# Kernel tuning notes

Measured on AMD Instinct MI355X. Metric: run time of the kernel, lower is better.

The kernel has to match this reference:

```python
import jax, jax.numpy as jnp
import numpy as np

N = 100000          # nodes
E = 1600000         # edges (avg degree 16)
D = 128             # prototype feature dim
C = 100             # num classes
NUM_LAYERS = 3      # propagation layers


def setup_inputs() -> dict:
    key = jax.random.key(0)
    k1, k2, k3, k4 = jax.random.split(key, 4)
    train_mask = jax.random.randint(k1, (N,), 0, 2) > 0                # bool [N]
    labels_all = jax.random.randint(k2, (N,), 0, C)                    # int   [N]
    edge_index = jax.random.randint(k3, (2, E), 0, N)                  # int   [2,E]
    global_protos = jax.random.normal(k4, (C, D), dtype=jnp.float32)   # [C,D]
    alpha = jnp.float32(0.5)                                           # learnable scalar
    return dict(train_mask=train_mask, global_protos=global_protos,
                labels_all=labels_all, edge_index=edge_index, alpha=alpha)


def _label_propagate(y0, edge_index, alpha):
    # symmetric GCN normalization D^-1/2 A D^-1/2 (no self loops), as in PyG LabelPropagation
    src, dst = edge_index[0], edge_index[1]
    deg = jax.ops.segment_sum(jnp.ones((E,), y0.dtype), dst, num_segments=N)
    deg_inv_sqrt = jnp.where(deg > 0, jax.lax.rsqrt(jnp.maximum(deg, 1.0)), 0.0)
    norm = deg_inv_sqrt[src] * deg_inv_sqrt[dst]                       # [E]
    res = (1.0 - alpha) * y0                                           # residual term
    out = y0
    for _ in range(NUM_LAYERS):
        msgs = out[src] * norm[:, None]                                # gather [E,D]
        agg = jax.ops.segment_sum(msgs, dst, num_segments=N)           # scatter-add [N,D]
        out = jnp.clip(alpha * agg + res, 0.0, 1.0)                    # post_step clamp
    return out


def reference(train_mask, global_protos, labels_all, edge_index, alpha):
    # proto_rep[train_mask] = global_protos[labels_all[train_mask]], zeros elsewhere
    y0 = jnp.where(train_mask[:, None], global_protos[labels_all], 0.0)  # [N,D]
    return _label_propagate(y0, edge_index, alpha)
```

## Files before the change

kernel.cpp:

```cpp
#include <hip/hip_runtime.h>
#include <stdint.h>

typedef _Float16 f16;

#define N_NODES 100000
#define N_EDGES 1600000
#define CAP     64
#define NC      196
#define SLOTS   40
#define SEGCAP  12288
#define EPB     4096
#define SPAD    (CAP + 4)


__global__ __launch_bounds__(256) void bin_kernel(
    const int* __restrict__ src, const int* __restrict__ dst,
    int* __restrict__ gcur, unsigned int* __restrict__ gbins) {
    __shared__ int lcnt[NC];
    __shared__ int gb[NC];
    __shared__ unsigned int lbuf[NC * SLOTS];
    int t = threadIdx.x;
    for (int b = t; b < NC; b += 256) lcnt[b] = 0;
    __syncthreads();

    int base = blockIdx.x * EPB;
    int sv[16], dv[16];
#pragma unroll
    for (int k = 0; k < 16; ++k) {
        int i = base + k * 256 + t;
        sv[k] = (i < N_EDGES) ? src[i] : -1;
        dv[k] = (i < N_EDGES) ? dst[i] : 0;
    }
#pragma unroll
    for (int k = 0; k < 16; ++k) {
        if (sv[k] >= 0) {
            int d = dv[k];
            int cb = d >> 9;
            unsigned rec = (unsigned)sv[k] | ((unsigned)(d & 511) << 17);
            int pos = atomicAdd(&lcnt[cb], 1);
            if (pos < SLOTS) {
                lbuf[cb * SLOTS + pos] = rec;
            } else {
                int gp = atomicAdd(&gcur[cb], 1);
                if (gp < SEGCAP) gbins[(size_t)cb * SEGCAP + gp] = rec;
            }
        }
    }
    __syncthreads();
    if (t < NC) {
        int c = lcnt[t]; if (c > SLOTS) c = SLOTS;
        gb[t] = atomicAdd(&gcur[t], c);
    }
    __syncthreads();
    int wave = t >> 6, lane = t & 63;
    for (int b = wave; b < NC; b += 4) {
        int c = lcnt[b]; if (c > SLOTS) c = SLOTS;
        if (lane < c)
            gbins[(size_t)b * SEGCAP + gb[b] + lane] = lbuf[b * SLOTS + lane];
    }
}


__global__ __launch_bounds__(512) void csr_kernel(
    const unsigned int* __restrict__ gbins, const int* __restrict__ gcur,
    int* __restrict__ cnt, int* __restrict__ csr, float* __restrict__ dis,
    const int* __restrict__ mask, const int* __restrict__ labels,
    int* __restrict__ c0, const float* __restrict__ protos,
    f16* __restrict__ pf16) {
    __shared__ int lc[512];
    int b = blockIdx.x;
    int t = threadIdx.x;
    lc[t] = 0;
    __syncthreads();
    int m = gcur[b]; if (m > SEGCAP) m = SEGCAP;
    const unsigned int* seg = gbins + (size_t)b * SEGCAP;
    int base = b << 9;
    for (int i = t; i < m; i += 512) {
        unsigned int v = seg[i];
        int dl = (int)(v >> 17);
        int pos = atomicAdd(&lc[dl], 1);
        if (pos < CAP) csr[(size_t)(base + dl) * CAP + pos] = (int)(v & 0x1FFFF);
    }
    __syncthreads();
    int n = base + t;
    if (n < N_NODES) {
        int d = lc[t];
        cnt[n] = d;
        dis[n] = (d > 0) ? rsqrtf((float)d) : 0.0f;
        c0[n] = mask[n] ? labels[n] : -1;
    }
    if (b < 25) pf16[b * 512 + t] = (f16)protos[b * 512 + t];
}


template <int MODE>
__global__ __launch_bounds__(256) void prop_kernel(
    const void* __restrict__ rows_, void* __restrict__ out,
    const int* __restrict__ cnt, const int* __restrict__ csr,
    const float* __restrict__ dis, const int* __restrict__ c0,
    const float* __restrict__ protos, const float* __restrict__ alpha_p) {
    __shared__ uint2 smeta[4][4][SPAD];
    int t = threadIdx.x;
    int wave = t >> 6, lane = t & 63;
    int grp = lane >> 4, s16 = lane & 15;
    int n = blockIdx.x * 16 + wave * 4 + grp;

    float alpha = *alpha_p;
    int m = cnt[n]; if (m > CAP) m = CAP;
    float dn = dis[n];
    const int* bucket = csr + (size_t)n * CAP;
    const float inv255 = 1.0f / 255.0f;

    int mm = m;
    { int o = __shfl_xor(mm, 16); mm = mm > o ? mm : o;
      o = __shfl_xor(mm, 32);     mm = mm > o ? mm : o; }
    int mp = (mm + 3) & ~3;

    for (int e = s16; e < mp; e += 16) {
        unsigned wb = 0, off = 0;
        if (e < m) {
            int s = bucket[e];
            float w = dis[s] * dn;
            if (MODE == 0) {
                int c = c0[s];
                if (c < 0) w = 0.f; else off = (unsigned)c << 4;
            } else {
                off = (unsigned)s << 4;
                w *= inv255;
            }
            wb = __float_as_uint(w);
        }
        smeta[wave][grp][e] = make_uint2(wb, off);
    }

    const uint4* md = (const uint4*)&smeta[wave][grp][0];
    float acc[8] = {0.f, 0.f, 0.f, 0.f, 0.f, 0.f, 0.f, 0.f};

    if (MODE == 0) {
        const uint4* r4 = (const uint4*)rows_;
        uint4 mA0, mA1, gA0, gA1, gA2, gA3;
        uint4 mB0, mB1, gB0, gB1, gB2, gB3;
#define LOADB(MM0, MM1, G0, G1, G2, G3, J) do {            \
    MM0 = md[(J) >> 1]; MM1 = md[((J) >> 1) + 1];          \
    G0 = r4[MM0.y + s16]; G1 = r4[MM0.w + s16];            \
    G2 = r4[MM1.y + s16]; G3 = r4[MM1.w + s16]; } while (0)
#define COMP1(WB, G) do {                                  \
    union { uint4 u; f16 h[8]; } q_; q_.u = (G);           \
    float w_ = __uint_as_float(WB);                        \
    _Pragma("unroll")                                      \
    for (int i_ = 0; i_ < 8; ++i_)                         \
        acc[i_] = fmaf((float)q_.h[i_], w_, acc[i_]); } while (0)
#define COMP(MM0, MM1, G0, G1, G2, G3) do {                \
    COMP1(MM0.x, G0); COMP1(MM0.z, G1);                    \
    COMP1(MM1.x, G2); COMP1(MM1.z, G3); } while (0)
        if (mp > 0) {
            LOADB(mA0, mA1, gA0, gA1, gA2, gA3, 0);
            for (int j = 0; j < mp; j += 8) {
                if (j + 4 < mp) LOADB(mB0, mB1, gB0, gB1, gB2, gB3, j + 4);
                COMP(mA0, mA1, gA0, gA1, gA2, gA3);
                if (j + 8 < mp) LOADB(mA0, mA1, gA0, gA1, gA2, gA3, j + 8);
                if (j + 4 < mp) COMP(mB0, mB1, gB0, gB1, gB2, gB3);
            }
        }
#undef LOADB
#undef COMP1
#undef COMP
    } else {
        const uint2* r2 = (const uint2*)rows_;
        uint4 mA0, mA1, mB0, mB1;
        uint2 gA0, gA1, gA2, gA3, gB0, gB1, gB2, gB3;
#define LOADB(MM0, MM1, G0, G1, G2, G3, J) do {            \
    MM0 = md[(J) >> 1]; MM1 = md[((J) >> 1) + 1];          \
    G0 = r2[MM0.y + s16]; G1 = r2[MM0.w + s16];            \
    G2 = r2[MM1.y + s16]; G3 = r2[MM1.w + s16]; } while (0)
#define COMP1(WB, G) do {                                  \
    float w_ = __uint_as_float(WB);                        \
    unsigned x_ = (G).x, y_ = (G).y;                       \
    acc[0] = fmaf((float)(x_ & 0xffu),         w_, acc[0]); \
    acc[1] = fmaf((float)((x_ >> 8) & 0xffu),  w_, acc[1]); \
    acc[2] = fmaf((float)((x_ >> 16) & 0xffu), w_, acc[2]); \
    acc[3] = fmaf((float)(x_ >> 24),           w_, acc[3]); \
    acc[4] = fmaf((float)(y_ & 0xffu),         w_, acc[4]); \
    acc[5] = fmaf((float)((y_ >> 8) & 0xffu),  w_, acc[5]); \
    acc[6] = fmaf((float)((y_ >> 16) & 0xffu), w_, acc[6]); \
    acc[7] = fmaf((float)(y_ >> 24),           w_, acc[7]); } while (0)
#define COMP(MM0, MM1, G0, G1, G2, G3) do {                \
    COMP1(MM0.x, G0); COMP1(MM0.z, G1);                    \
    COMP1(MM1.x, G2); COMP1(MM1.z, G3); } while (0)
        if (mp > 0) {
            LOADB(mA0, mA1, gA0, gA1, gA2, gA3, 0);
            for (int j = 0; j < mp; j += 8) {
                if (j + 4 < mp) LOADB(mB0, mB1, gB0, gB1, gB2, gB3, j + 4);
                COMP(mA0, mA1, gA0, gA1, gA2, gA3);
                if (j + 8 < mp) LOADB(mA0, mA1, gA0, gA1, gA2, gA3, j + 8);
                if (j + 4 < mp) COMP(mB0, mB1, gB0, gB1, gB2, gB3);
            }
        }
#undef LOADB
#undef COMP1
#undef COMP
    }

    int cn = c0[n];
    float ra = 1.f - alpha;
    float y[8] = {0.f, 0.f, 0.f, 0.f, 0.f, 0.f, 0.f, 0.f};
    if (cn >= 0) {
        const float4* pr = (const float4*)(protos + (size_t)cn * 128) + (s16 << 1);
        float4 p0 = pr[0], p1 = pr[1];
        y[0] = p0.x; y[1] = p0.y; y[2] = p0.z; y[3] = p0.w;
        y[4] = p1.x; y[5] = p1.y; y[6] = p1.z; y[7] = p1.w;
    }
    float o[8];
#pragma unroll
    for (int i = 0; i < 8; ++i)
        o[i] = fminf(fmaxf(fmaf(alpha, acc[i], ra * y[i]), 0.f), 1.f);

    if (MODE == 2) {
        float4* dst = (float4*)out + ((size_t)n << 5) + (s16 << 1);
        dst[0] = make_float4(o[0], o[1], o[2], o[3]);
        dst[1] = make_float4(o[4], o[5], o[6], o[7]);
    } else {
        unsigned q[8];
#pragma unroll
        for (int i = 0; i < 8; ++i) q[i] = (unsigned)(o[i] * 255.f + 0.5f);
        unsigned lo = q[0] | (q[1] << 8) | (q[2] << 16) | (q[3] << 24);
        unsigned hi = q[4] | (q[5] << 8) | (q[6] << 16) | (q[7] << 24);
        ((uint2*)out)[((size_t)n << 4) + s16] = make_uint2(lo, hi);
    }
}


extern "C" void kernel_launch(void* const* d_in, const int* in_sizes, int n_in,
                              void* d_out, int out_size, void* d_ws, size_t ws_size,
                              hipStream_t stream) {
    const int*   mask   = (const int*)d_in[0];
    const float* protos = (const float*)d_in[1];
    const int*   labels = (const int*)d_in[2];
    const int*   ei     = (const int*)d_in[3];
    const float* alpha  = (const float*)d_in[4];
    const int* src = ei;
    const int* dst = ei + N_EDGES;

    int*          gcur  = (int*)d_ws;
    int*          cnt   = gcur + 256;
    float*        dis   = (float*)(cnt + N_NODES);
    int*          c0    = (int*)(dis + N_NODES);
    int*          csr   = c0 + N_NODES;
    f16*          pf16  = (f16*)(csr + (size_t)N_NODES * CAP);
    unsigned char* region = (unsigned char*)(pf16 + 16384);
    unsigned int* gbins = (unsigned int*)region;
    uint8_t*      bufA  = (uint8_t*)region;
    uint8_t*      bufB  = bufA + (size_t)N_NODES * 128;

    hipMemsetAsync(gcur, 0, 256 * sizeof(int), stream);

    int bgrid = (N_EDGES + EPB - 1) / EPB;
    bin_kernel<<<bgrid, 256, 0, stream>>>(src, dst, gcur, gbins);
    csr_kernel<<<NC, 512, 0, stream>>>(gbins, gcur, cnt, csr, dis,
                                       mask, labels, c0, protos, pf16);

    int pgrid = N_NODES / 16;
    prop_kernel<0><<<pgrid, 256, 0, stream>>>(pf16, bufA, cnt, csr, dis, c0,
                                              protos, alpha);
    prop_kernel<1><<<pgrid, 256, 0, stream>>>(bufA, bufB, cnt, csr, dis, c0,
                                              protos, alpha);
    prop_kernel<2><<<pgrid, 256, 0, stream>>>(bufB, d_out, cnt, csr, dis, c0,
                                              protos, alpha);
}
```

Measured before the change: 228.3 us.

## Precompute per-edge weights in layer 0 and coalesce CSR writes via LDS

The CSR build now runs four blocks per bin, each staging its 128 destination rows in shared memory and writing them out as coalesced uint4 stores. It also emits a packed (deg_inv_sqrt, class) meta array. The first propagation layer reads that packed meta and writes a per-edge (src, weight) record array. Later layers then read one int2 per edge instead of gathering dis[src] randomly. The cost is an extra 8-byte-per-edge write in layer 0, and each csr block rescans its whole bin segment four times.

```diff
diff --git a/kernel.cpp b/kernel.cpp
--- a/kernel.cpp
+++ b/kernel.cpp
@@ -65,39 +65,65 @@
     const unsigned int* __restrict__ gbins, const int* __restrict__ gcur,
     int* __restrict__ cnt, int* __restrict__ csr, float* __restrict__ dis,
     const int* __restrict__ mask, const int* __restrict__ labels,
-    int* __restrict__ c0, const float* __restrict__ protos,
-    f16* __restrict__ pf16) {
-    __shared__ int lc[512];
-    int b = blockIdx.x;
+    int* __restrict__ c0, int2* __restrict__ meta,
+    const float* __restrict__ protos, f16* __restrict__ pf16) {
+    __shared__ int lc[128];
+    __shared__ int rows[128][CAP];
+    int cb = blockIdx.x >> 2;
+    int sb = blockIdx.x & 3;
     int t = threadIdx.x;
-    lc[t] = 0;
-    __syncthreads();
-    int m = gcur[b]; if (m > SEGCAP) m = SEGCAP;
-    const unsigned int* seg = gbins + (size_t)b * SEGCAP;
-    int base = b << 9;
+    if (t < 128) lc[t] = 0;
+    __syncthreads();
+    int m = gcur[cb]; if (m > SEGCAP) m = SEGCAP;
+    const unsigned int* seg = gbins + (size_t)cb * SEGCAP;
+    int base = (cb << 9) + (sb << 7);
     for (int i = t; i < m; i += 512) {
-        unsigned int v = seg[i];
+        unsigned v = seg[i];
         int dl = (int)(v >> 17);
-        int pos = atomicAdd(&lc[dl], 1);
-        if (pos < CAP) csr[(size_t)(base + dl) * CAP + pos] = (int)(v & 0x1FFFF);
-    }
-    __syncthreads();
-    int n = base + t;
-    if (n < N_NODES) {
-        int d = lc[t];
-        cnt[n] = d;
-        dis[n] = (d > 0) ? rsqrtf((float)d) : 0.0f;
-        c0[n] = mask[n] ? labels[n] : -1;
-    }
-    if (b < 25) pf16[b * 512 + t] = (f16)protos[b * 512 + t];
-}
-
-
-template <int MODE>
-__global__ __launch_bounds__(256) void prop_kernel(
-    const void* __restrict__ rows_, void* __restrict__ out,
+        if ((dl >> 7) == sb) {
+            int local = dl & 127;
+            int pos = atomicAdd(&lc[local], 1);
+            if (pos < CAP) rows[local][pos] = (int)(v & 0x1FFFF);
+        }
+    }
+    __syncthreads();
+    if (t < 128) {
+        int n = base + t;
+        if (n < N_NODES) {
+            int d = lc[t];
+            cnt[n] = d;
+            float dv = (d > 0) ? rsqrtf((float)d) : 0.0f;
+            dis[n] = dv;
+            int c = mask[n] ? labels[n] : -1;
+            c0[n] = c;
+            meta[n] = make_int2(__float_as_int(dv), c);
+        }
+    }
+    uint4* csr4 = (uint4*)csr;
+    for (int idx = t; idx < 128 * 16; idx += 512) {
+        int node = idx >> 4, ch = idx & 15;
+        int n = base + node;
+        if (n < N_NODES) {
+            int d = lc[node]; if (d > CAP) d = CAP;
+            if (ch * 4 < d) {
+                uint4 w;
+                w.x = (unsigned)rows[node][ch * 4 + 0];
+                w.y = (unsigned)rows[node][ch * 4 + 1];
+                w.z = (unsigned)rows[node][ch * 4 + 2];
+                w.w = (unsigned)rows[node][ch * 4 + 3];
+                csr4[(size_t)n * 16 + ch] = w;
+            }
+        }
+    }
+    if (blockIdx.x < 25) pf16[blockIdx.x * 512 + t] = (f16)protos[blockIdx.x * 512 + t];
+}
+
+
+__global__ __launch_bounds__(256) void prop0_kernel(
+    const f16* __restrict__ pf16, uint8_t* __restrict__ out,
     const int* __restrict__ cnt, const int* __restrict__ csr,
     const float* __restrict__ dis, const int* __restrict__ c0,
+    const int2* __restrict__ meta, int2* __restrict__ csr2,
     const float* __restrict__ protos, const float* __restrict__ alpha_p) {
     __shared__ uint2 smeta[4][4][SPAD];
     int t = threadIdx.x;
@@ -109,7 +135,7 @@
     int m = cnt[n]; if (m > CAP) m = CAP;
     float dn = dis[n];
     const int* bucket = csr + (size_t)n * CAP;
-    const float inv255 = 1.0f / 255.0f;
+    int2* bucket2 = csr2 + (size_t)n * CAP;
 
     int mm = m;
     { int o = __shfl_xor(mm, 16); mm = mm > o ? mm : o;
@@ -120,26 +146,21 @@
         unsigned wb = 0, off = 0;
         if (e < m) {
             int s = bucket[e];
-            float w = dis[s] * dn;
-            if (MODE == 0) {
-                int c = c0[s];
-                if (c < 0) w = 0.f; else off = (unsigned)c << 4;
-            } else {
-                off = (unsigned)s << 4;
-                w *= inv255;
-            }
-            wb = __float_as_uint(w);
+            int2 mt = meta[s];
+            float wpre = __int_as_float(mt.x) * dn;
+            bucket2[e] = make_int2(s, __float_as_int(wpre));
+            int c = mt.y;
+            if (c >= 0) { wb = __float_as_uint(wpre); off = (unsigned)c << 4; }
         }
         smeta[wave][grp][e] = make_uint2(wb, off);
     }
 
     const uint4* md = (const uint4*)&smeta[wave][grp][0];
+    const uint4* r4 = (const uint4*)pf16;
     float acc[8] = {0.f, 0.f, 0.f, 0.f, 0.f, 0.f, 0.f, 0.f};
 
-    if (MODE == 0) {
-        const uint4* r4 = (const uint4*)rows_;
-        uint4 mA0, mA1, gA0, gA1, gA2, gA3;
-        uint4 mB0, mB1, gB0, gB1, gB2, gB3;
+    uint4 mA0, mA1, gA0, gA1, gA2, gA3;
+    uint4 mB0, mB1, gB0, gB1, gB2, gB3;
 #define LOADB(MM0, MM1, G0, G1, G2, G3, J) do {            \
     MM0 = md[(J) >> 1]; MM1 = md[((J) >> 1) + 1];          \
     G0 = r4[MM0.y + s16]; G1 = r4[MM0.w + s16];            \
@@ -153,22 +174,78 @@
 #define COMP(MM0, MM1, G0, G1, G2, G3) do {                \
     COMP1(MM0.x, G0); COMP1(MM0.z, G1);                    \
     COMP1(MM1.x, G2); COMP1(MM1.z, G3); } while (0)
-        if (mp > 0) {
-            LOADB(mA0, mA1, gA0, gA1, gA2, gA3, 0);
-            for (int j = 0; j < mp; j += 8) {
-                if (j + 4 < mp) LOADB(mB0, mB1, gB0, gB1, gB2, gB3, j + 4);
-                COMP(mA0, mA1, gA0, gA1, gA2, gA3);
-                if (j + 8 < mp) LOADB(mA0, mA1, gA0, gA1, gA2, gA3, j + 8);
-                if (j + 4 < mp) COMP(mB0, mB1, gB0, gB1, gB2, gB3);
-            }
-        }
+    if (mp > 0) {
+        LOADB(mA0, mA1, gA0, gA1, gA2, gA3, 0);
+        for (int j = 0; j < mp; j += 8) {
+            if (j + 4 < mp) LOADB(mB0, mB1, gB0, gB1, gB2, gB3, j + 4);
+            COMP(mA0, mA1, gA0, gA1, gA2, gA3);
+            if (j + 8 < mp) LOADB(mA0, mA1, gA0, gA1, gA2, gA3, j + 8);
+            if (j + 4 < mp) COMP(mB0, mB1, gB0, gB1, gB2, gB3);
+        }
+    }
 #undef LOADB
 #undef COMP1
 #undef COMP
-    } else {
-        const uint2* r2 = (const uint2*)rows_;
-        uint4 mA0, mA1, mB0, mB1;
-        uint2 gA0, gA1, gA2, gA3, gB0, gB1, gB2, gB3;
+
+    int cn = c0[n];
+    float ra = 1.f - alpha;
+    float y[8] = {0.f, 0.f, 0.f, 0.f, 0.f, 0.f, 0.f, 0.f};
+    if (cn >= 0) {
+        const float4* pr = (const float4*)(protos + (size_t)cn * 128) + (s16 << 1);
+        float4 p0 = pr[0], p1 = pr[1];
+        y[0] = p0.x; y[1] = p0.y; y[2] = p0.z; y[3] = p0.w;
+        y[4] = p1.x; y[5] = p1.y; y[6] = p1.z; y[7] = p1.w;
+    }
+    unsigned q[8];
+#pragma unroll
+    for (int i = 0; i < 8; ++i) {
+        float o = fminf(fmaxf(fmaf(alpha, acc[i], ra * y[i]), 0.f), 1.f);
+        q[i] = (unsigned)(o * 255.f + 0.5f);
+    }
+    unsigned lo = q[0] | (q[1] << 8) | (q[2] << 16) | (q[3] << 24);
+    unsigned hi = q[4] | (q[5] << 8) | (q[6] << 16) | (q[7] << 24);
+    ((uint2*)out)[((size_t)n << 4) + s16] = make_uint2(lo, hi);
+}
+
+
+template <int MODE>
+__global__ __launch_bounds__(256) void prop_kernel(
+    const uint8_t* __restrict__ rows_, void* __restrict__ out,
+    const int* __restrict__ cnt, const int2* __restrict__ csr2,
+    const int* __restrict__ c0,
+    const float* __restrict__ protos, const float* __restrict__ alpha_p) {
+    __shared__ uint2 smeta[4][4][SPAD];
+    int t = threadIdx.x;
+    int wave = t >> 6, lane = t & 63;
+    int grp = lane >> 4, s16 = lane & 15;
+    int n = blockIdx.x * 16 + wave * 4 + grp;
+
+    float alpha = *alpha_p;
+    int m = cnt[n]; if (m > CAP) m = CAP;
+    const int2* bucket2 = csr2 + (size_t)n * CAP;
+    const float inv255 = 1.0f / 255.0f;
+
+    int mm = m;
+    { int o = __shfl_xor(mm, 16); mm = mm > o ? mm : o;
+      o = __shfl_xor(mm, 32);     mm = mm > o ? mm : o; }
+    int mp = (mm + 3) & ~3;
+
+    for (int e = s16; e < mp; e += 16) {
+        unsigned wb = 0, off = 0;
+        if (e < m) {
+            int2 rec = bucket2[e];
+            off = (unsigned)rec.x << 4;
+            wb = __float_as_uint(__int_as_float(rec.y) * inv255);
+        }
+        smeta[wave][grp][e] = make_uint2(wb, off);
+    }
+
+    const uint4* md = (const uint4*)&smeta[wave][grp][0];
+    const uint2* r2 = (const uint2*)rows_;
+    float acc[8] = {0.f, 0.f, 0.f, 0.f, 0.f, 0.f, 0.f, 0.f};
+
+    uint4 mA0, mA1, mB0, mB1;
+    uint2 gA0, gA1, gA2, gA3, gB0, gB1, gB2, gB3;
 #define LOADB(MM0, MM1, G0, G1, G2, G3, J) do {            \
     MM0 = md[(J) >> 1]; MM1 = md[((J) >> 1) + 1];          \
     G0 = r2[MM0.y + s16]; G1 = r2[MM0.w + s16];            \
@@ -187,19 +264,18 @@
 #define COMP(MM0, MM1, G0, G1, G2, G3) do {                \
     COMP1(MM0.x, G0); COMP1(MM0.z, G1);                    \
     COMP1(MM1.x, G2); COMP1(MM1.z, G3); } while (0)
-        if (mp > 0) {
-            LOADB(mA0, mA1, gA0, gA1, gA2, gA3, 0);
-            for (int j = 0; j < mp; j += 8) {
-                if (j + 4 < mp) LOADB(mB0, mB1, gB0, gB1, gB2, gB3, j + 4);
-                COMP(mA0, mA1, gA0, gA1, gA2, gA3);
-                if (j + 8 < mp) LOADB(mA0, mA1, gA0, gA1, gA2, gA3, j + 8);
-                if (j + 4 < mp) COMP(mB0, mB1, gB0, gB1, gB2, gB3);
-            }
-        }
+    if (mp > 0) {
+        LOADB(mA0, mA1, gA0, gA1, gA2, gA3, 0);
+        for (int j = 0; j < mp; j += 8) {
+            if (j + 4 < mp) LOADB(mB0, mB1, gB0, gB1, gB2, gB3, j + 4);
+            COMP(mA0, mA1, gA0, gA1, gA2, gA3);
+            if (j + 8 < mp) LOADB(mA0, mA1, gA0, gA1, gA2, gA3, j + 8);
+            if (j + 4 < mp) COMP(mB0, mB1, gB0, gB1, gB2, gB3);
+        }
+    }
 #undef LOADB
 #undef COMP1
 #undef COMP
-    }
 
     int cn = c0[n];
     float ra = 1.f - alpha;
@@ -245,8 +321,10 @@
     int*          cnt   = gcur + 256;
     float*        dis   = (float*)(cnt + N_NODES);
     int*          c0    = (int*)(dis + N_NODES);
-    int*          csr   = c0 + N_NODES;
-    f16*          pf16  = (f16*)(csr + (size_t)N_NODES * CAP);
+    int2*         meta  = (int2*)(c0 + N_NODES);
+    int*          csr   = (int*)(meta + N_NODES);
+    int2*         csr2  = (int2*)(csr + (size_t)N_NODES * CAP);
+    f16*          pf16  = (f16*)(csr2 + (size_t)N_NODES * CAP);
     unsigned char* region = (unsigned char*)(pf16 + 16384);
     unsigned int* gbins = (unsigned int*)region;
     uint8_t*      bufA  = (uint8_t*)region;
@@ -256,14 +334,14 @@
 
     int bgrid = (N_EDGES + EPB - 1) / EPB;
     bin_kernel<<<bgrid, 256, 0, stream>>>(src, dst, gcur, gbins);
-    csr_kernel<<<NC, 512, 0, stream>>>(gbins, gcur, cnt, csr, dis,
-                                       mask, labels, c0, protos, pf16);
+    csr_kernel<<<NC * 4, 512, 0, stream>>>(gbins, gcur, cnt, csr, dis,
+                                           mask, labels, c0, meta, protos, pf16);
 
     int pgrid = N_NODES / 16;
-    prop_kernel<0><<<pgrid, 256, 0, stream>>>(pf16, bufA, cnt, csr, dis, c0,
+    prop0_kernel<<<pgrid, 256, 0, stream>>>(pf16, bufA, cnt, csr, dis, c0,
+                                            meta, csr2, protos, alpha);
+    prop_kernel<1><<<pgrid, 256, 0, stream>>>(bufA, bufB, cnt, csr2, c0,
                                               protos, alpha);
-    prop_kernel<1><<<pgrid, 256, 0, stream>>>(bufA, bufB, cnt, csr, dis, c0,
+    prop_kernel<2><<<pgrid, 256, 0, stream>>>(bufB, d_out, cnt, csr2, c0,
                                               protos, alpha);
-    prop_kernel<2><<<pgrid, 256, 0, stream>>>(bufB, d_out, cnt, csr, dis, c0,
-                                              protos, alpha);
-}
+}
```

Measured after the change: 218.9 us. -4.1%, faster.
